# Performance work log

Measured on AMD Instinct MI355X. Metric: run time of the kernel, lower is better.

Reference implementation:

```python
import jax, jax.numpy as jnp
import numpy as np
from jax import lax

B = 65536

def _conv(x, w, b):
    y = lax.conv_general_dilated(x, w, (1, 1), 'VALID',
                                 dimension_numbers=('NCHW', 'OIHW', 'NCHW'))
    return y + b[None, :, None, None]

def _maxpool2(x):
    return lax.reduce_window(x, -jnp.inf, lax.max, (1, 1, 2, 2), (1, 1, 2, 2), 'VALID')

def _cnot01(s):  # control wire0, target wire1; s: [B,2,2] indexed [b,q0,q1]
    return jnp.stack([s[:, 0, :], s[:, 1, ::-1]], axis=1)

def _cnot10(s):  # control wire1, target wire0
    return jnp.stack([s[:, :, 0], s[:, ::-1, 1]], axis=2)

def _ry(half_angle):  # RY(2*half_angle) as used in circuit (theta/2 = half_angle)
    c, si = jnp.cos(half_angle), jnp.sin(half_angle)
    return jnp.stack([jnp.stack([c, -si]), jnp.stack([si, c])]).astype(jnp.complex64)

def _apply_w0(s, U):
    return jnp.einsum('ij,bjk->bik', U, s)

def _apply_w1(s, U):
    return jnp.einsum('ij,bkj->bki', U, s)

def _quantum(x2, p):
    # x2: [B,2] float32, p: [8] float32. Batched 2-qubit statevector sim.
    x0, x1 = x2[:, 0], x2[:, 1]
    n = x2.shape[0]
    s = jnp.full((n, 2, 2), 0.5 + 0.0j, dtype=jnp.complex64)  # H|0> x H|0>
    # RZ(2*x0) on wire 0: diag(e^{-i x0}, e^{i x0})
    s = s * jnp.exp(1j * jnp.stack([-x0, x0], axis=1).astype(jnp.complex64))[:, :, None]
    # RZ(2*x1) on wire 1
    s = s * jnp.exp(1j * jnp.stack([-x1, x1], axis=1).astype(jnp.complex64))[:, None, :]
    s = _cnot01(s)
    ang = (jnp.pi - x0) * (jnp.pi - x1)  # RZ(2*ang) on wire 1
    s = s * jnp.exp(1j * jnp.stack([-ang, ang], axis=1).astype(jnp.complex64))[:, None, :]
    s = _cnot01(s)
    s = _apply_w0(s, _ry(p[0])); s = _apply_w1(s, _ry(p[1])); s = _cnot01(s)
    s = _apply_w0(s, _ry(p[2])); s = _apply_w1(s, _ry(p[3])); s = _cnot10(s)
    s = _apply_w0(s, _ry(p[4])); s = _apply_w1(s, _ry(p[5])); s = _cnot01(s)
    s = _apply_w0(s, _ry(p[6])); s = _apply_w1(s, _ry(p[7]))
    z = jnp.array([[1.0, -1.0], [-1.0, 1.0]], dtype=jnp.float32)  # Z0 (x) Z1 signs
    prob = (s.real ** 2 + s.imag ** 2)
    return jnp.sum(prob * z[None], axis=(1, 2))  # [B]

def setup_inputs() -> dict:
    key = jax.random.key(0)
    ks = jax.random.split(key, 12)
    d = {}
    d['x'] = jax.random.normal(ks[0], (B, 1, 28, 28), dtype=jnp.float32)
    d['conv1_w'] = jax.random.normal(ks[1], (2, 1, 5, 5), dtype=jnp.float32) * 0.2
    d['conv1_b'] = jax.random.normal(ks[2], (2,), dtype=jnp.float32) * 0.1
    d['conv2_w'] = jax.random.normal(ks[3], (16, 2, 5, 5), dtype=jnp.float32) * 0.14
    d['conv2_b'] = jax.random.normal(ks[4], (16,), dtype=jnp.float32) * 0.1
    d['fc1_w'] = jax.random.normal(ks[5], (64, 256), dtype=jnp.float32) * 0.0625
    d['fc1_b'] = jax.random.normal(ks[6], (64,), dtype=jnp.float32) * 0.05
    d['fc2_w'] = jax.random.normal(ks[7], (2, 64), dtype=jnp.float32) * 0.125
    d['fc2_b'] = jax.random.normal(ks[8], (2,), dtype=jnp.float32) * 0.05
    d['fc3_w'] = jax.random.normal(ks[9], (1, 1), dtype=jnp.float32)
    d['fc3_b'] = jax.random.normal(ks[10], (1,), dtype=jnp.float32) * 0.05
    d['qnn_params'] = jax.random.uniform(ks[11], (8,), dtype=jnp.float32)
    return d

def reference(x, conv1_w, conv1_b, conv2_w, conv2_b, fc1_w, fc1_b,
              fc2_w, fc2_b, fc3_w, fc3_b, qnn_params):
    h = jax.nn.relu(_conv(x, conv1_w, conv1_b))        # [B,2,24,24]
    h = _maxpool2(h)                                    # [B,2,12,12]
    h = jax.nn.relu(_conv(h, conv2_w, conv2_b))        # [B,16,8,8]
    h = _maxpool2(h)                                    # [B,16,4,4]
    # Dropout2d: identity in eval mode
    h = h.reshape(h.shape[0], -1)                       # [B,256]
    h = jax.nn.relu(h @ fc1_w.T + fc1_b)                # [B,64]
    h = h @ fc2_w.T + fc2_b                             # [B,2]
    q = _quantum(h, qnn_params)[:, None]                # [B,1]
    y = q @ fc3_w.T + fc3_b                             # [B,1]
    logits = jnp.concatenate([y, 1.0 - y], axis=-1)     # [B,2]
    return jax.nn.log_softmax(logits, axis=1)
```

## Files before the change

kernel.cpp:

```cpp
#include <hip/hip_runtime.h>
#include <math.h>


typedef float v2f __attribute__((ext_vector_type(2)));
typedef float v4f __attribute__((ext_vector_type(4)));

static __device__ __forceinline__ v2f vfma2(v2f a, float w, v2f c) {
    return __builtin_elementwise_fma(a, (v2f){w, w}, c);
}
static __device__ __forceinline__ v2f vmax2(v2f a, v2f b) {
    return __builtin_elementwise_max(a, b);
}

#define PK_FMA_W0(acc, w, xp) \
    asm("v_pk_fma_f32 %0, %1, %2, %0 op_sel:[0,0,0] op_sel_hi:[1,0,1]" \
        : "+v"(acc) : "s"(w), "v"(xp))
#define PK_FMA_W1(acc, w, xp) \
    asm("v_pk_fma_f32 %0, %1, %2, %0 op_sel:[0,1,0] op_sel_hi:[1,1,1]" \
        : "+v"(acc) : "s"(w), "v"(xp))

#define P1_PAIR 580
#define HB_OC   36
#define HB_PAIR 576
#define W2_OC   60

__global__ __launch_bounds__(256, 5)
void hqcnn_fused(const float* __restrict__ x,
                 const float* __restrict__ w1,
                 const float* __restrict__ b1,
                 const float* __restrict__ w2,
                 const float* __restrict__ b2,
                 const float* __restrict__ fw1,
                 const float* __restrict__ fb1,
                 const float* __restrict__ fw2,
                 const float* __restrict__ fb2,
                 const float* __restrict__ fw3,
                 const float* __restrict__ fb3,
                 const float* __restrict__ qp,
                 float* __restrict__ out)
{
    __shared__ __align__(16) float p1s[4 * P1_PAIR];
    __shared__ __align__(16) float hb[4 * HB_PAIR];
    __shared__ __align__(16) float w2s[16 * W2_OC];

    const int t = threadIdx.x;
    const int wv = t >> 6;
    const int lane = t & 63;
    const long base = (long)blockIdx.x * 8;

    for (int f = t; f < 800; f += 256) {
        int oc = f / 50;
        int rem = f - oc * 50;
        int c = rem >= 25;
        int k = rem - c * 25;
        w2s[oc * W2_OC + c * 28 + k] = w2[f];
    }
    __syncthreads();

    {
        v2f w1p[25];
        #pragma unroll
        for (int k = 0; k < 25; ++k)
            w1p[k] = (v2f){w1[k], w1[25 + k]};
        const v2f bias1 = (v2f){b1[0], b1[1]};

        #pragma unroll
        for (int it = 0; it < 2; ++it) {
            int f = lane + it * 64;
            if (f < 96) {
                int s = f / 48;
                int r = f - s * 48;
                int i = r >> 2, jh = r & 3;
                const float* xrow = x + (base + 2 * wv + s) * 784;
                v2f acc[12];
                #pragma unroll
                for (int q = 0; q < 12; ++q) acc[q] = (v2f){0.f, 0.f};
                #pragma unroll
                for (int u = 0; u < 6; ++u) {
                    const v2f* xp = (const v2f*)(xrow + (2 * i + u) * 28 + 6 * jh);
                    v2f P[5] = { xp[0], xp[1], xp[2], xp[3], xp[4] };
                    #pragma unroll
                    for (int a = 0; a < 2; ++a) {
                        if (a <= u && (u - a) <= 4) {
                            const int wu = u - a;
                            #pragma unroll
                            for (int v = 0; v < 5; ++v) {
                                #pragma unroll
                                for (int j = 0; j < 6; ++j) {
                                    const int e = j + v;
                                    if (e & 1) { PK_FMA_W1(acc[a * 6 + j], w1p[wu * 5 + v], P[e >> 1]); }
                                    else       { PK_FMA_W0(acc[a * 6 + j], w1p[wu * 5 + v], P[e >> 1]); }
                                }
                            }
                        }
                    }
                }
                #pragma unroll
                for (int m = 0; m < 3; ++m) {
                    v2f mx = vmax2(vmax2(acc[2 * m], acc[2 * m + 1]),
                                   vmax2(acc[6 + 2 * m], acc[7 + 2 * m]));
                    mx = mx + bias1;
                    mx = vmax2(mx, (v2f){0.f, 0.f});
                    int pc = 3 * jh + m;
                    int off = wv * P1_PAIR + 2 * (i * 12 + pc) + s;
                    p1s[off] = mx.x;
                    p1s[off + 288] = mx.y;
                }
            }
        }
    }
    asm volatile("s_waitcnt lgkmcnt(0)" ::: "memory");

    {
        int oc = (lane >> 2) & 15;
        int qi = (lane >> 1) & 1;
        int qj = lane & 1;
        v2f acc[16];
        #pragma unroll
        for (int q = 0; q < 16; ++q) acc[q] = (v2f){0.f, 0.f};
        #pragma unroll
        for (int c = 0; c < 2; ++c) {
            float wvv[28];
            {
                const v4f* wp = (const v4f*)w2s + oc * (W2_OC / 4) + c * 7;
                #pragma unroll
                for (int j = 0; j < 7; ++j) {
                    v4f w4 = wp[j];
                    wvv[j*4+0] = w4.x; wvv[j*4+1] = w4.y; wvv[j*4+2] = w4.z; wvv[j*4+3] = w4.w;
                }
            }
            #pragma unroll
            for (int u = 0; u < 8; ++u) {
                int rb = wv * (P1_PAIR / 4) + c * 72 + (4 * qi + u) * 6 + 2 * qj;
                v4f q0 = ((const v4f*)p1s)[rb + 0];
                v4f q1 = ((const v4f*)p1s)[rb + 1];
                v4f q2 = ((const v4f*)p1s)[rb + 2];
                v4f q3 = ((const v4f*)p1s)[rb + 3];
                v2f rr[8] = { {q0.x,q0.y},{q0.z,q0.w},{q1.x,q1.y},{q1.z,q1.w},
                              {q2.x,q2.y},{q2.z,q2.w},{q3.x,q3.y},{q3.z,q3.w} };
                #pragma unroll
                for (int a = 0; a < 4; ++a) {
                    if (a <= u && (u - a) <= 4) {
                        const int wu = u - a;
                        #pragma unroll
                        for (int b = 0; b < 4; ++b) {
                            v2f s0 = acc[a * 4 + b];
                            #pragma unroll
                            for (int v = 0; v < 5; ++v)
                                s0 = vfma2(rr[b + v], wvv[wu * 5 + v], s0);
                            acc[a * 4 + b] = s0;
                        }
                    }
                }
            }
        }
        float bias = b2[oc];
        #pragma unroll
        for (int a2 = 0; a2 < 2; ++a2)
            #pragma unroll
            for (int b2i = 0; b2i < 2; ++b2i) {
                v2f m = vmax2(vmax2(acc[(2*a2)*4 + 2*b2i],     acc[(2*a2)*4 + 2*b2i + 1]),
                              vmax2(acc[(2*a2+1)*4 + 2*b2i], acc[(2*a2+1)*4 + 2*b2i + 1]));
                m = m + (v2f){bias, bias};
                m = vmax2(m, (v2f){0.f, 0.f});
                int pos = (2*qi + a2) * 4 + (2*qj + b2i);
                ((v2f*)hb)[wv * (HB_PAIR / 2) + oc * (HB_OC / 2) + pos] = m;
            }
    }
    __syncthreads();

    {
        const v4f* wrow = (const v4f*)(fw1 + lane * 256 + wv * 64);
        v2f part[4];
        #pragma unroll
        for (int p = 0; p < 4; ++p) part[p] = (v2f){0.f, 0.f};
        #pragma unroll
        for (int jo = 0; jo < 4; ++jo) {
            int oc = wv * 4 + jo;
            #pragma unroll
            for (int jj = 0; jj < 4; ++jj) {
                v4f w4 = wrow[jo * 4 + jj];
                #pragma unroll
                for (int p = 0; p < 4; ++p) {
                    const v4f* hp = (const v4f*)(hb + p * HB_PAIR + oc * HB_OC + jj * 8);
                    v4f hA = hp[0], hB = hp[1];
                    part[p] = vfma2((v2f){hA.x, hA.y}, w4.x, part[p]);
                    part[p] = vfma2((v2f){hA.z, hA.w}, w4.y, part[p]);
                    part[p] = vfma2((v2f){hB.x, hB.y}, w4.z, part[p]);
                    part[p] = vfma2((v2f){hB.z, hB.w}, w4.w, part[p]);
                }
            }
        }
        v2f* pb = (v2f*)p1s;
        #pragma unroll
        for (int p = 0; p < 4; ++p)
            pb[(wv * 4 + p) * 64 + lane] = part[p];
    }
    __syncthreads();

    {
        const v2f* pb = (const v2f*)p1s;
        float fb = fb1[lane];
        v2f acc = (v2f){fb, fb};
        acc = acc + pb[(0 * 4 + wv) * 64 + lane];
        acc = acc + pb[(1 * 4 + wv) * 64 + lane];
        acc = acc + pb[(2 * 4 + wv) * 64 + lane];
        acc = acc + pb[(3 * 4 + wv) * 64 + lane];
        v2f a2 = vmax2(acc, (v2f){0.f, 0.f});

        float w20 = fw2[lane], w21 = fw2[64 + lane];
        v2f pz0 = a2 * (v2f){w20, w20};
        v2f pz1 = a2 * (v2f){w21, w21};
        #pragma unroll
        for (int off = 32; off > 0; off >>= 1) {
            pz0.x += __shfl_xor(pz0.x, off, 64);
            pz0.y += __shfl_xor(pz0.y, off, 64);
            pz1.x += __shfl_xor(pz1.x, off, 64);
            pz1.y += __shfl_xor(pz1.y, off, 64);
        }
        int h = lane >> 5;
        float x0 = (h ? pz0.y : pz0.x) + fb2[0];
        float x1 = (h ? pz1.y : pz1.x) + fb2[1];

        float sr[4], si[4];
        {
            float th0 = -x0 - x1, th1 = -x0 + x1, th2 = x0 - x1, th3 = x0 + x1;
            sr[0] = 0.5f * __cosf(th0); si[0] = 0.5f * __sinf(th0);
            sr[1] = 0.5f * __cosf(th1); si[1] = 0.5f * __sinf(th1);
            sr[2] = 0.5f * __cosf(th2); si[2] = 0.5f * __sinf(th2);
            sr[3] = 0.5f * __cosf(th3); si[3] = 0.5f * __sinf(th3);
        }
        {
            float tr = sr[2]; sr[2] = sr[3]; sr[3] = tr;
            float ti = si[2]; si[2] = si[3]; si[3] = ti;
            float ang = ((float)M_PI - x0) * ((float)M_PI - x1);
            float ca = __cosf(ang), sa = __sinf(ang);
            float r, im;
            r = sr[0]; im = si[0]; sr[0] = r*ca + im*sa; si[0] = im*ca - r*sa;
            r = sr[2]; im = si[2]; sr[2] = r*ca + im*sa; si[2] = im*ca - r*sa;
            r = sr[1]; im = si[1]; sr[1] = r*ca - im*sa; si[1] = im*ca + r*sa;
            r = sr[3]; im = si[3]; sr[3] = r*ca - im*sa; si[3] = im*ca + r*sa;
            tr = sr[2]; sr[2] = sr[3]; sr[3] = tr;
            ti = si[2]; si[2] = si[3]; si[3] = ti;
        }
        float cp[8], sp[8];
        #pragma unroll
        for (int g = 0; g < 8; ++g) { float q = qp[g]; cp[g] = __cosf(q); sp[g] = __sinf(q); }

        #define QRY0(cc, ss) { \
            float a0r=sr[0], a0i=si[0], a1r=sr[2], a1i=si[2]; \
            sr[0]=cc*a0r-ss*a1r; si[0]=cc*a0i-ss*a1i; \
            sr[2]=ss*a0r+cc*a1r; si[2]=ss*a0i+cc*a1i; \
            float b0r=sr[1], b0i=si[1], b1r=sr[3], b1i=si[3]; \
            sr[1]=cc*b0r-ss*b1r; si[1]=cc*b0i-ss*b1i; \
            sr[3]=ss*b0r+cc*b1r; si[3]=ss*b0i+cc*b1i; }
        #define QRY1(cc, ss) { \
            float a0r=sr[0], a0i=si[0], a1r=sr[1], a1i=si[1]; \
            sr[0]=cc*a0r-ss*a1r; si[0]=cc*a0i-ss*a1i; \
            sr[1]=ss*a0r+cc*a1r; si[1]=ss*a0i+cc*a1i; \
            float b0r=sr[2], b0i=si[2], b1r=sr[3], b1i=si[3]; \
            sr[2]=cc*b0r-ss*b1r; si[2]=cc*b0i-ss*b1i; \
            sr[3]=ss*b0r+cc*b1r; si[3]=ss*b0i+cc*b1i; }
        #define QSWAP(i_, j_) { float tr=sr[i_]; sr[i_]=sr[j_]; sr[j_]=tr; \
                                float ti=si[i_]; si[i_]=si[j_]; si[j_]=ti; }

        QRY0(cp[0], sp[0]);
        QRY1(cp[1], sp[1]);
        QSWAP(2, 3);
        QRY0(cp[2], sp[2]);
        QRY1(cp[3], sp[3]);
        QSWAP(1, 3);
        QRY0(cp[4], sp[4]);
        QRY1(cp[5], sp[5]);
        QSWAP(2, 3);
        QRY0(cp[6], sp[6]);
        QRY1(cp[7], sp[7]);

        float qv = (sr[0]*sr[0] + si[0]*si[0])
                 - (sr[1]*sr[1] + si[1]*si[1])
                 - (sr[2]*sr[2] + si[2]*si[2])
                 + (sr[3]*sr[3] + si[3]*si[3]);
        float y = fmaf(qv, fw3[0], fb3[0]);
        float l0 = y, l1 = 1.0f - y;
        float m = fmaxf(l0, l1);
        float lse = m + __logf(__expf(l0 - m) + __expf(l1 - m));
        int lk = lane & 31;
        if (lk < 2) {
            float o = (lk == 0) ? (l0 - lse) : (l1 - lse);
            out[(base + 2 * wv + h) * 2 + lk] = o;
        }
        #undef QRY0
        #undef QRY1
        #undef QSWAP
    }
}

extern "C" void kernel_launch(void* const* d_in, const int* in_sizes, int n_in,
                              void* d_out, int out_size, void* d_ws, size_t ws_size,
                              hipStream_t stream) {
    const float* x   = (const float*)d_in[0];
    const float* w1  = (const float*)d_in[1];
    const float* b1  = (const float*)d_in[2];
    const float* w2  = (const float*)d_in[3];
    const float* b2  = (const float*)d_in[4];
    const float* fw1 = (const float*)d_in[5];
    const float* fb1 = (const float*)d_in[6];
    const float* fw2 = (const float*)d_in[7];
    const float* fb2 = (const float*)d_in[8];
    const float* fw3 = (const float*)d_in[9];
    const float* fb3 = (const float*)d_in[10];
    const float* qp  = (const float*)d_in[11];
    float* outp = (float*)d_out;

    int B = in_sizes[0] / 784;
    int nblk = B / 8;
    hipLaunchKernelGGL(hqcnn_fused, dim3(nblk), dim3(256), 0, stream,
                       x, w1, b1, w2, b2, fw1, fb1, fw2, fb2, fw3, fb3, qp, outp);
}
```

Baseline: 413.6 us.

## Move conv2 and fc1 onto bf16x3 MFMA with split hi/lo weights

Conv2 (as an im2col GEMM) and fc1 are moved from packed FP32 FMAs onto 16x16x32 bf16 MFMA instructions. Each fp32 operand is split into hi and lo bf16 halves, and three MFMAs are issued per tile to keep roughly fp32 accuracy. A small prep kernel converts w2 and fc1 weights into hi/lo bf16 tables in the workspace on every call. Shared-memory layouts, the pooling/reduction epilogues and the fc2 reduction are rebuilt around the MFMA tile layout, and occupancy hints are raised. The trade-offs are extra VALU work for packing activations, gather-style LDS reads for im2col, and an additional kernel launch.

```diff
diff --git a/kernel.cpp b/kernel.cpp
--- a/kernel.cpp
+++ b/kernel.cpp
@@ -3,7 +3,10 @@
 
 
 typedef float v2f __attribute__((ext_vector_type(2)));
-typedef float v4f __attribute__((ext_vector_type(4)));
+typedef float f32x4 __attribute__((ext_vector_type(4)));
+typedef short bf16x8 __attribute__((ext_vector_type(8)));
+
+union B8 { unsigned int u[4]; bf16x8 v; };
 
 static __device__ __forceinline__ v2f vfma2(v2f a, float w, v2f c) {
     return __builtin_elementwise_fma(a, (v2f){w, w}, c);
@@ -19,43 +22,78 @@
     asm("v_pk_fma_f32 %0, %1, %2, %0 op_sel:[0,1,0] op_sel_hi:[1,1,1]" \
         : "+v"(acc) : "s"(w), "v"(xp))
 
-#define P1_PAIR 580
-#define HB_OC   36
-#define HB_PAIR 576
-#define W2_OC   60
-
-__global__ __launch_bounds__(256, 5)
+#define MFMA16(a, b, c) __builtin_amdgcn_mfma_f32_16x16x32_bf16(a, b, c, 0, 0, 0)
+
+static __device__ __forceinline__ void pack_hilo(const float* f, bf16x8& bh, bf16x8& bl) {
+    B8 H, L;
+    #pragma unroll
+    for (int jp = 0; jp < 4; ++jp) {
+        unsigned int u0 = __float_as_uint(f[2 * jp]);
+        unsigned int u1 = __float_as_uint(f[2 * jp + 1]);
+        H.u[jp] = (u1 & 0xFFFF0000u) | (u0 >> 16);
+        float l0 = f[2 * jp]     - __uint_as_float(u0 & 0xFFFF0000u);
+        float l1 = f[2 * jp + 1] - __uint_as_float(u1 & 0xFFFF0000u);
+        L.u[jp] = (__float_as_uint(l1) & 0xFFFF0000u) | (__float_as_uint(l0) >> 16);
+    }
+    bh = H.v; bl = L.v;
+}
+
+#define A2_HI 0
+#define A2_LO 1024
+#define A1_HI 2048
+#define A1_LO (2048 + 16384)
+
+#define P1_S 292
+#define HB_S 260
+
+__global__ __launch_bounds__(256)
+void hqcnn_prep(const float* __restrict__ w2, const float* __restrict__ fw1,
+                unsigned short* __restrict__ ws) {
+    int t = blockIdx.x * 256 + threadIdx.x;
+    if (blockIdx.x == 0) {
+        for (int e = threadIdx.x; e < 1024; e += 256) {
+            int m = e >> 6, k = e & 63;
+            int c = k >> 5, uv = k & 31;
+            float val = (uv < 25) ? w2[m * 50 + c * 25 + uv] : 0.f;
+            unsigned int u = __float_as_uint(val);
+            float lo = val - __uint_as_float(u & 0xFFFF0000u);
+            ws[A2_HI + e] = (unsigned short)(u >> 16);
+            ws[A2_LO + e] = (unsigned short)(__float_as_uint(lo) >> 16);
+        }
+    }
+    for (int e = t; e < 16384; e += gridDim.x * 256) {
+        float val = fw1[e];
+        unsigned int u = __float_as_uint(val);
+        float lo = val - __uint_as_float(u & 0xFFFF0000u);
+        ws[A1_HI + e] = (unsigned short)(u >> 16);
+        ws[A1_LO + e] = (unsigned short)(__float_as_uint(lo) >> 16);
+    }
+}
+
+__global__ __launch_bounds__(256, 6)
 void hqcnn_fused(const float* __restrict__ x,
                  const float* __restrict__ w1,
                  const float* __restrict__ b1,
-                 const float* __restrict__ w2,
                  const float* __restrict__ b2,
-                 const float* __restrict__ fw1,
                  const float* __restrict__ fb1,
                  const float* __restrict__ fw2,
                  const float* __restrict__ fb2,
                  const float* __restrict__ fw3,
                  const float* __restrict__ fb3,
                  const float* __restrict__ qp,
+                 const unsigned short* __restrict__ ws,
                  float* __restrict__ out)
 {
-    __shared__ __align__(16) float p1s[4 * P1_PAIR];
-    __shared__ __align__(16) float hb[4 * HB_PAIR];
-    __shared__ __align__(16) float w2s[16 * W2_OC];
+    __shared__ __align__(16) float p1s[8 * P1_S];
+    __shared__ __align__(16) float hbs[8 * HB_S];
+    __shared__ __align__(16) float zbuf[4 * 32];
 
     const int t = threadIdx.x;
     const int wv = t >> 6;
     const int lane = t & 63;
+    const int n = lane & 15;
+    const int q = lane >> 4;
     const long base = (long)blockIdx.x * 8;
-
-    for (int f = t; f < 800; f += 256) {
-        int oc = f / 50;
-        int rem = f - oc * 50;
-        int c = rem >= 25;
-        int k = rem - c * 25;
-        w2s[oc * W2_OC + c * 28 + k] = w2[f];
-    }
-    __syncthreads();
 
     {
         v2f w1p[25];
@@ -74,7 +112,7 @@
                 const float* xrow = x + (base + 2 * wv + s) * 784;
                 v2f acc[12];
                 #pragma unroll
-                for (int q = 0; q < 12; ++q) acc[q] = (v2f){0.f, 0.f};
+                for (int qq = 0; qq < 12; ++qq) acc[qq] = (v2f){0.f, 0.f};
                 #pragma unroll
                 for (int u = 0; u < 6; ++u) {
                     const v2f* xp = (const v2f*)(xrow + (2 * i + u) * 28 + 6 * jh);
@@ -102,9 +140,9 @@
                     mx = mx + bias1;
                     mx = vmax2(mx, (v2f){0.f, 0.f});
                     int pc = 3 * jh + m;
-                    int off = wv * P1_PAIR + 2 * (i * 12 + pc) + s;
+                    int off = (2 * wv + s) * P1_S + i * 12 + pc;
                     p1s[off] = mx.x;
-                    p1s[off + 288] = mx.y;
+                    p1s[off + 144] = mx.y;
                 }
             }
         }
@@ -112,115 +150,111 @@
     asm volatile("s_waitcnt lgkmcnt(0)" ::: "memory");
 
     {
-        int oc = (lane >> 2) & 15;
-        int qi = (lane >> 1) & 1;
-        int qj = lane & 1;
-        v2f acc[16];
-        #pragma unroll
-        for (int q = 0; q < 16; ++q) acc[q] = (v2f){0.f, 0.f};
-        #pragma unroll
-        for (int c = 0; c < 2; ++c) {
-            float wvv[28];
-            {
-                const v4f* wp = (const v4f*)w2s + oc * (W2_OC / 4) + c * 7;
-                #pragma unroll
-                for (int j = 0; j < 7; ++j) {
-                    v4f w4 = wp[j];
-                    wvv[j*4+0] = w4.x; wvv[j*4+1] = w4.y; wvv[j*4+2] = w4.z; wvv[j*4+3] = w4.w;
+        const bf16x8* A2h = (const bf16x8*)(ws + A2_HI);
+        const bf16x8* A2l = (const bf16x8*)(ws + A2_LO);
+        bf16x8 a_h0 = A2h[n * 8 + q],     a_h1 = A2h[n * 8 + 4 + q];
+        bf16x8 a_l0 = A2l[n * 8 + q],     a_l1 = A2l[n * 8 + 4 + q];
+
+        int offs[8]; bool vld[8];
+        #pragma unroll
+        for (int j = 0; j < 8; ++j) {
+            int uv = q * 8 + j;
+            int u = (uv * 205) >> 10;
+            int v = uv - u * 5;
+            bool ok = uv < 25;
+            offs[j] = ok ? (u * 12 + v) : 0;
+            vld[j] = ok;
+        }
+        f32x4 bias4 = *(const f32x4*)(b2 + q * 4);
+
+        for (int t8 = 0; t8 < 8; ++t8) {
+            int smp = 2 * wv + (t8 >> 2);
+            int tt = t8 & 3;
+            int prow = 2 * tt + (n >> 3);
+            int pcol = n & 7;
+            f32x4 acc = {0.f, 0.f, 0.f, 0.f};
+            #pragma unroll
+            for (int c = 0; c < 2; ++c) {
+                int pb = smp * P1_S + c * 144 + prow * 12 + pcol;
+                float fv[8];
+                #pragma unroll
+                for (int j = 0; j < 8; ++j) {
+                    float xv = p1s[pb + offs[j]];
+                    fv[j] = vld[j] ? xv : 0.f;
+                }
+                bf16x8 bh, bl;
+                pack_hilo(fv, bh, bl);
+                bf16x8 ah = c ? a_h1 : a_h0;
+                bf16x8 al = c ? a_l1 : a_l0;
+                acc = MFMA16(ah, bh, acc);
+                acc = MFMA16(ah, bl, acc);
+                acc = MFMA16(al, bh, acc);
+            }
+            #pragma unroll
+            for (int r = 0; r < 4; ++r) {
+                float vmx = acc[r];
+                vmx = fmaxf(vmx, __shfl_xor(vmx, 1, 64));
+                vmx = fmaxf(vmx, __shfl_xor(vmx, 8, 64));
+                float pv = fmaxf(vmx + bias4[r], 0.f);
+                if ((n & 1) == 0 && n < 8) {
+                    int jc = n >> 1;
+                    hbs[smp * HB_S + (q * 4 + r) * 16 + tt * 4 + jc] = pv;
                 }
             }
-            #pragma unroll
-            for (int u = 0; u < 8; ++u) {
-                int rb = wv * (P1_PAIR / 4) + c * 72 + (4 * qi + u) * 6 + 2 * qj;
-                v4f q0 = ((const v4f*)p1s)[rb + 0];
-                v4f q1 = ((const v4f*)p1s)[rb + 1];
-                v4f q2 = ((const v4f*)p1s)[rb + 2];
-                v4f q3 = ((const v4f*)p1s)[rb + 3];
-                v2f rr[8] = { {q0.x,q0.y},{q0.z,q0.w},{q1.x,q1.y},{q1.z,q1.w},
-                              {q2.x,q2.y},{q2.z,q2.w},{q3.x,q3.y},{q3.z,q3.w} };
-                #pragma unroll
-                for (int a = 0; a < 4; ++a) {
-                    if (a <= u && (u - a) <= 4) {
-                        const int wu = u - a;
-                        #pragma unroll
-                        for (int b = 0; b < 4; ++b) {
-                            v2f s0 = acc[a * 4 + b];
-                            #pragma unroll
-                            for (int v = 0; v < 5; ++v)
-                                s0 = vfma2(rr[b + v], wvv[wu * 5 + v], s0);
-                            acc[a * 4 + b] = s0;
-                        }
-                    }
-                }
+        }
+    }
+    __syncthreads();
+
+    {
+        const bf16x8* A1h = (const bf16x8*)(ws + A1_HI);
+        const bf16x8* A1l = (const bf16x8*)(ws + A1_LO);
+        const int abase = (wv * 16 + n) * 32 + q;
+        f32x4 acc = {0.f, 0.f, 0.f, 0.f};
+        #pragma unroll
+        for (int kk = 0; kk < 8; ++kk) {
+            bf16x8 ah = A1h[abase + kk * 4];
+            bf16x8 al = A1l[abase + kk * 4];
+            float fv[8];
+            if (n < 8) {
+                const f32x4* hp = (const f32x4*)(hbs + n * HB_S + kk * 32 + q * 8);
+                f32x4 h0 = hp[0], h1 = hp[1];
+                fv[0] = h0.x; fv[1] = h0.y; fv[2] = h0.z; fv[3] = h0.w;
+                fv[4] = h1.x; fv[5] = h1.y; fv[6] = h1.z; fv[7] = h1.w;
+            } else {
+                #pragma unroll
+                for (int j = 0; j < 8; ++j) fv[j] = 0.f;
             }
-        }
-        float bias = b2[oc];
-        #pragma unroll
-        for (int a2 = 0; a2 < 2; ++a2)
-            #pragma unroll
-            for (int b2i = 0; b2i < 2; ++b2i) {
-                v2f m = vmax2(vmax2(acc[(2*a2)*4 + 2*b2i],     acc[(2*a2)*4 + 2*b2i + 1]),
-                              vmax2(acc[(2*a2+1)*4 + 2*b2i], acc[(2*a2+1)*4 + 2*b2i + 1]));
-                m = m + (v2f){bias, bias};
-                m = vmax2(m, (v2f){0.f, 0.f});
-                int pos = (2*qi + a2) * 4 + (2*qj + b2i);
-                ((v2f*)hb)[wv * (HB_PAIR / 2) + oc * (HB_OC / 2) + pos] = m;
-            }
+            bf16x8 bh, bl;
+            pack_hilo(fv, bh, bl);
+            acc = MFMA16(ah, bh, acc);
+            acc = MFMA16(ah, bl, acc);
+            acc = MFMA16(al, bh, acc);
+        }
+        f32x4 fb4 = *(const f32x4*)(fb1 + wv * 16 + q * 4);
+        f32x4 w20 = *(const f32x4*)(fw2 + wv * 16 + q * 4);
+        f32x4 w21 = *(const f32x4*)(fw2 + 64 + wv * 16 + q * 4);
+        float p0 = 0.f, p1v = 0.f;
+        #pragma unroll
+        for (int r = 0; r < 4; ++r) {
+            float a = fmaxf(acc[r] + fb4[r], 0.f);
+            p0  = fmaf(a, w20[r], p0);
+            p1v = fmaf(a, w21[r], p1v);
+        }
+        p0  += __shfl_xor(p0, 16, 64);  p0  += __shfl_xor(p0, 32, 64);
+        p1v += __shfl_xor(p1v, 16, 64); p1v += __shfl_xor(p1v, 32, 64);
+        if (q == 0) {
+            zbuf[wv * 32 + n * 2]     = p0;
+            zbuf[wv * 32 + n * 2 + 1] = p1v;
+        }
     }
     __syncthreads();
 
     {
-        const v4f* wrow = (const v4f*)(fw1 + lane * 256 + wv * 64);
-        v2f part[4];
-        #pragma unroll
-        for (int p = 0; p < 4; ++p) part[p] = (v2f){0.f, 0.f};
-        #pragma unroll
-        for (int jo = 0; jo < 4; ++jo) {
-            int oc = wv * 4 + jo;
-            #pragma unroll
-            for (int jj = 0; jj < 4; ++jj) {
-                v4f w4 = wrow[jo * 4 + jj];
-                #pragma unroll
-                for (int p = 0; p < 4; ++p) {
-                    const v4f* hp = (const v4f*)(hb + p * HB_PAIR + oc * HB_OC + jj * 8);
-                    v4f hA = hp[0], hB = hp[1];
-                    part[p] = vfma2((v2f){hA.x, hA.y}, w4.x, part[p]);
-                    part[p] = vfma2((v2f){hA.z, hA.w}, w4.y, part[p]);
-                    part[p] = vfma2((v2f){hB.x, hB.y}, w4.z, part[p]);
-                    part[p] = vfma2((v2f){hB.z, hB.w}, w4.w, part[p]);
-                }
-            }
-        }
-        v2f* pb = (v2f*)p1s;
-        #pragma unroll
-        for (int p = 0; p < 4; ++p)
-            pb[(wv * 4 + p) * 64 + lane] = part[p];
-    }
-    __syncthreads();
-
-    {
-        const v2f* pb = (const v2f*)p1s;
-        float fb = fb1[lane];
-        v2f acc = (v2f){fb, fb};
-        acc = acc + pb[(0 * 4 + wv) * 64 + lane];
-        acc = acc + pb[(1 * 4 + wv) * 64 + lane];
-        acc = acc + pb[(2 * 4 + wv) * 64 + lane];
-        acc = acc + pb[(3 * 4 + wv) * 64 + lane];
-        v2f a2 = vmax2(acc, (v2f){0.f, 0.f});
-
-        float w20 = fw2[lane], w21 = fw2[64 + lane];
-        v2f pz0 = a2 * (v2f){w20, w20};
-        v2f pz1 = a2 * (v2f){w21, w21};
-        #pragma unroll
-        for (int off = 32; off > 0; off >>= 1) {
-            pz0.x += __shfl_xor(pz0.x, off, 64);
-            pz0.y += __shfl_xor(pz0.y, off, 64);
-            pz1.x += __shfl_xor(pz1.x, off, 64);
-            pz1.y += __shfl_xor(pz1.y, off, 64);
-        }
-        int h = lane >> 5;
-        float x0 = (h ? pz0.y : pz0.x) + fb2[0];
-        float x1 = (h ? pz1.y : pz1.x) + fb2[1];
+        int s = t & 7;
+        float x0 = fb2[0] + zbuf[s * 2]     + zbuf[32 + s * 2]
+                          + zbuf[64 + s * 2] + zbuf[96 + s * 2];
+        float x1 = fb2[1] + zbuf[s * 2 + 1] + zbuf[32 + s * 2 + 1]
+                          + zbuf[64 + s * 2 + 1] + zbuf[96 + s * 2 + 1];
 
         float sr[4], si[4];
         {
@@ -245,7 +279,7 @@
         }
         float cp[8], sp[8];
         #pragma unroll
-        for (int g = 0; g < 8; ++g) { float q = qp[g]; cp[g] = __cosf(q); sp[g] = __sinf(q); }
+        for (int g = 0; g < 8; ++g) { float qv = qp[g]; cp[g] = __cosf(qv); sp[g] = __sinf(qv); }
 
         #define QRY0(cc, ss) { \
             float a0r=sr[0], a0i=si[0], a1r=sr[2], a1i=si[2]; \
@@ -284,10 +318,9 @@
         float l0 = y, l1 = 1.0f - y;
         float m = fmaxf(l0, l1);
         float lse = m + __logf(__expf(l0 - m) + __expf(l1 - m));
-        int lk = lane & 31;
-        if (lk < 2) {
-            float o = (lk == 0) ? (l0 - lse) : (l1 - lse);
-            out[(base + 2 * wv + h) * 2 + lk] = o;
+        if (t < 16) {
+            int comp = t >> 3;
+            out[(base + s) * 2 + comp] = comp ? (l1 - lse) : (l0 - lse);
         }
         #undef QRY0
         #undef QRY1
@@ -311,9 +344,12 @@
     const float* fb3 = (const float*)d_in[10];
     const float* qp  = (const float*)d_in[11];
     float* outp = (float*)d_out;
+    unsigned short* wsp = (unsigned short*)d_ws;
+
+    hipLaunchKernelGGL(hqcnn_prep, dim3(64), dim3(256), 0, stream, w2, fw1, wsp);
 
     int B = in_sizes[0] / 784;
     int nblk = B / 8;
     hipLaunchKernelGGL(hqcnn_fused, dim3(nblk), dim3(256), 0, stream,
-                       x, w1, b1, w2, b2, fw1, fb1, fw2, fb2, fw3, fb3, qp, outp);
-}
+                       x, w1, b1, b2, fb1, fw2, fb2, fw3, fb3, qp, wsp, outp);
+}
```

After: 399.0 us. 1.04x faster.
